# Optimization experiments

Hardware: AMD Instinct MI355X
Metric: run time of the kernel (lower is better)

## Reference

```python
import jax, jax.numpy as jnp
import numpy as np

H = 16      # num_head
DH = 64     # d_head
D = H * DH  # d_model
NEG = -10000.0


def _proj(x, W, b):
    # torch Linear: y = x @ W^T + b
    return jnp.einsum('bld,od->blo', x, W) + b


def _heads(x):
    b, l, _ = x.shape
    return x.reshape(b, l, H, DH)


def _attn_logits(feat_q, mask_q, feat_k, mask_k, Wq, bq, Wk, bk):
    q = _heads(_proj(feat_q, Wq, bq))   # b lq h dh
    k = _heads(_proj(feat_k, Wk, bk))   # b lk h dh
    logits = jnp.einsum('bqhd,bkhd->bhqk', q, k)
    m = mask_q[:, None, :, None] & mask_k[:, None, None, :]  # b 1 lq lk
    return jnp.where(m, logits, NEG)


def setup_inputs() -> dict:
    key = jax.random.key(0)
    ks = jax.random.split(key, 12)
    B, Lv, Lt = 4, 1024, 256
    scale = 1.0 / np.sqrt(D).astype(np.float32)
    inp = {
        'vid_feat': jax.random.normal(ks[0], (B, Lv, D), jnp.float32),
        'vid_mask': jax.random.bernoulli(ks[1], 0.9, (B, Lv)),
        'txt_feat': jax.random.normal(ks[2], (B, Lt, D), jnp.float32),
        'txt_mask': jax.random.bernoulli(ks[3], 0.9, (B, Lt)),
    }
    names = ['v2v', 't2v', 'v2t', 't2t']
    for i, n in enumerate(names):
        inp['W_' + n] = jax.random.normal(ks[4 + i], (3, D, D), jnp.float32) * scale
        inp['b_' + n] = jax.random.normal(ks[8 + i], (3, D), jnp.float32) * 0.01
    return inp


def reference(vid_feat, vid_mask, txt_feat, txt_mask,
              W_v2v, b_v2v, W_t2v, b_t2v, W_v2t, b_v2t, W_t2t, b_t2t):
    B, Lv, _ = vid_feat.shape
    B, Lt, _ = txt_feat.shape
    # sr_ratio == 1: vid_feat_sr == vid_feat, vid_mask_sr == vid_mask
    vid_feat_sr, vid_mask_sr = vid_feat, vid_mask

    # values (proj index 2), concatenated along key length
    v_value = jnp.concatenate([_proj(vid_feat_sr, W_v2v[2], b_v2v[2]),
                               _proj(txt_feat, W_t2v[2], b_t2v[2])], axis=1)
    v_value = _heads(v_value)  # b (Lv+Lt) h dh
    t_value = jnp.concatenate([_proj(vid_feat_sr, W_v2t[2], b_v2t[2]),
                               _proj(txt_feat, W_t2t[2], b_t2t[2])], axis=1)
    t_value = _heads(t_value)

    v2v = _attn_logits(vid_feat, vid_mask, vid_feat_sr, vid_mask_sr,
                       W_v2v[0], b_v2v[0], W_v2v[1], b_v2v[1])
    t2v = _attn_logits(vid_feat, vid_mask, txt_feat, txt_mask,
                       W_t2v[0], b_t2v[0], W_t2v[1], b_t2v[1])
    v2t = _attn_logits(txt_feat, txt_mask, vid_feat_sr, vid_mask_sr,
                       W_v2t[0], b_v2t[0], W_v2t[1], b_v2t[1])
    t2t = _attn_logits(txt_feat, txt_mask, txt_feat, txt_mask,
                       W_t2t[0], b_t2t[0], W_t2t[1], b_t2t[1])

    v_logits = jnp.concatenate([v2v, t2v], axis=-1)  # b h Lv (Lv+Lt)
    t_logits = jnp.concatenate([v2t, t2t], axis=-1)  # b h Lt (Lv+Lt)
    inv_sqrt_dh = jnp.float32(1.0 / np.sqrt(DH))

    # NOTE: original applies softmax, THEN divides by sqrt(d_head) (faithful)
    vid_out = jnp.einsum('bhqk,bkhd->bqhd',
                         jax.nn.softmax(v_logits, axis=-1) * inv_sqrt_dh,
                         v_value).reshape(B, Lv, D)
    txt_out = jnp.einsum('bhqk,bkhd->bqhd',
                         jax.nn.softmax(t_logits, axis=-1) * inv_sqrt_dh,
                         t_value).reshape(B, Lt, D)
    return vid_out, txt_out
```

## Files before the change

### kernel.cpp

```cpp
#include <hip/hip_runtime.h>


typedef __attribute__((ext_vector_type(8))) _Float16  half8;
typedef __attribute__((ext_vector_type(4))) _Float16  half4;
typedef __attribute__((ext_vector_type(4))) float     f32x4;
typedef __attribute__((ext_vector_type(4))) unsigned int uint4v;
typedef __attribute__((ext_vector_type(2))) unsigned int uint2v;

#define MFMA_F16   __builtin_amdgcn_mfma_f32_16x16x32_f16
#define MFMA16_F16 __builtin_amdgcn_mfma_f32_16x16x16f16

static __device__ __forceinline__ unsigned short f_to_f16u(float f) {
  _Float16 h = (_Float16)f;
  return __builtin_bit_cast(unsigned short, h);
}

#define GLOAD_LDS16(g, l)                                            \
  __builtin_amdgcn_global_load_lds(                                  \
      (const __attribute__((address_space(1))) void*)(g),            \
      (__attribute__((address_space(3))) void*)(l), 16, 0, 0)

struct CvtDesc { const float* src; unsigned short* dst; int n8; };
struct CvtArgs { CvtDesc d[14]; };

__global__ __launch_bounds__(256) void cvt_fp16(CvtArgs ca) {
  const CvtDesc dd = ca.d[blockIdx.y];
  const int stride = gridDim.x * blockDim.x;
  for (int i = blockIdx.x * blockDim.x + threadIdx.x; i < dd.n8; i += stride) {
    const f32x4 a = ((const f32x4*)dd.src)[i * 2];
    const f32x4 b = ((const f32x4*)dd.src)[i * 2 + 1];
    half8 h;
    h[0] = (_Float16)a[0]; h[1] = (_Float16)a[1];
    h[2] = (_Float16)a[2]; h[3] = (_Float16)a[3];
    h[4] = (_Float16)b[0]; h[5] = (_Float16)b[1];
    h[6] = (_Float16)b[2]; h[7] = (_Float16)b[3];
    ((half8*)dd.dst)[i] = h;
  }
}

__global__ __launch_bounds__(256) void make_kbias(
    const int* __restrict__ vmask, const int* __restrict__ tmask,
    float* __restrict__ kb) {
  const int b = blockIdx.y;
  const int k = blockIdx.x * 256 + threadIdx.x;
  if (k >= 1280) return;
  const int m = (k < 1024) ? vmask[b * 1024 + k] : tmask[b * 256 + k - 1024];
  kb[b * 1280 + k] = m ? 0.0f : -10000.0f;
}

static __device__ __forceinline__ void copy_out_tile(
    const unsigned short* Cs, unsigned short* dst, int tid,
    int b, int l0, int h0, int Ld, int soff, int mode) {
  for (int i = 0; i < 8; ++i) {
    const int c     = i * 256 + tid;
    const int major = c >> 4;
    const int kc    = c & 15;
    if (mode == 1) {
      const int base = (kc >> 2) * 32 + (kc & 3) * 4;
      const int sw   = major & 7;
      const int o1   = major * 136 + (((base >> 3) ^ sw) << 3) + (base & 7);
      const int b2   = base + 16;
      const int o2   = major * 136 + (((b2 >> 3) ^ sw) << 3) + (b2 & 7);
      const uint2v lo = *(const uint2v*)&Cs[o1];
      const uint2v hi = *(const uint2v*)&Cs[o2];
      uint4v val; val[0] = lo[0]; val[1] = lo[1]; val[2] = hi[0]; val[3] = hi[1];
      const int hh = h0 + (major >> 6);
      const int dh = major & 63;
      const int k  = soff + l0 + (kc >> 2) * 32;
      const size_t el = (size_t)(b * 16 + hh) * 81920 + (size_t)(k >> 5) * 2048 +
                        dh * 32 + (kc & 3) * 8;
      *(uint4v*)(dst + el) = val;
    } else {
      const uint4v val =
          *(const uint4v*)&Cs[major * 136 + ((kc ^ (major & 7)) << 3)];
      if (mode == 0) {
        const size_t el =
            ((size_t)(b * 16 + h0 + (kc >> 3)) * Ld + soff + l0 + major) * 64 +
            (kc & 7) * 8;
        *(uint4v*)(dst + el) = val;
      } else {
        const int k   = soff + l0 + major;
        const int dh0 = (kc & 7) * 8;
        const size_t el = (size_t)(b * 16 + h0 + (kc >> 3)) * 81920 +
                          (size_t)(k >> 4) * 1024 + (dh0 >> 5) * 512 +
                          (k & 15) * 32 + ((dh0 >> 3) & 3) * 8;
        *(uint4v*)(dst + el) = val;
      }
    }
  }
}

struct ProjDescH {
  const unsigned short* X;
  const unsigned short* W;
  const float* Bv;
  unsigned short* dst;
  int M, lxsh, Ld, soff, mode;
};
struct ProjArgsH { ProjDescH d[12]; };

__global__ __launch_bounds__(256) void proj_gemm_h(ProjArgsH pa) {
  const ProjDescH dd = pa.d[blockIdx.z];
  const int m0 = blockIdx.y * 128;
  if (m0 >= dd.M) return;
  const int n0 = blockIdx.x * 128;

  __shared__ __align__(16) unsigned char smem[34816];
  unsigned short* As = (unsigned short*)smem;
  unsigned short* Bs = As + 4096;
  unsigned short* Cs = (unsigned short*)smem;

  const int tid  = threadIdx.x;
  const int lane = tid & 63;
  const int w    = tid >> 6;
  const int wr   = (w >> 1) * 64;
  const int wc   = (w & 1) * 64;
  const int ql   = lane & 15;
  const int qd   = lane >> 4;

  f32x4 acc[4][4];
  for (int i = 0; i < 4; ++i)
    for (int j = 0; j < 4; ++j) acc[i][j] = (f32x4)(0.0f);

  const unsigned short* Xg = dd.X + (size_t)m0 * 1024;
  const unsigned short* Wg = dd.W + (size_t)n0 * 1024;

  for (int k0 = 0; k0 < 1024; k0 += 32) {
    __syncthreads();
    for (int half = 0; half < 2; ++half) {
      const int cb  = w * 128 + half * 64;
      const int c   = cb + lane;
      const int row = c >> 2;
      const int kcg = (c & 3) ^ (row & 3);
      GLOAD_LDS16(Xg + row * 1024 + k0 + kcg * 8, As + cb * 8);
      GLOAD_LDS16(Wg + row * 1024 + k0 + kcg * 8, Bs + cb * 8);
    }
    __syncthreads();

    half8 af[4], bf[4];
    for (int mt = 0; mt < 4; ++mt) {
      const int row = wr + mt * 16 + ql;
      af[mt] = *(const half8*)&As[row * 32 + ((qd ^ (row & 3)) << 3)];
    }
    for (int nt = 0; nt < 4; ++nt) {
      const int row = wc + nt * 16 + ql;
      bf[nt] = *(const half8*)&Bs[row * 32 + ((qd ^ (row & 3)) << 3)];
    }
    for (int mt = 0; mt < 4; ++mt)
      for (int nt = 0; nt < 4; ++nt)
        acc[mt][nt] = MFMA_F16(af[mt], bf[nt], acc[mt][nt], 0, 0, 0);
  }

  float bv[4];
  for (int nt = 0; nt < 4; ++nt)
    bv[nt] = dd.Bv[n0 + wc + nt * 16 + ql];

  __syncthreads();

  for (int mt = 0; mt < 4; ++mt) {
    for (int nt = 0; nt < 4; ++nt) {
      const int nl = wc + nt * 16 + ql;
      for (int r = 0; r < 4; ++r) {
        const int ml = wr + mt * 16 + qd * 4 + r;
        const int row = dd.mode == 1 ? nl : ml;
        const int col = dd.mode == 1 ? ml : nl;
        const float v = acc[mt][nt][r] + bv[nt];
        Cs[row * 136 + (((col >> 3) ^ (row & 7)) << 3) + (col & 7)] = f_to_f16u(v);
      }
    }
  }
  __syncthreads();

  copy_out_tile(Cs, dd.dst, tid, m0 >> dd.lxsh, m0 & ((1 << dd.lxsh) - 1),
                n0 >> 6, dd.Ld, dd.soff, dd.mode);
}

struct ProjDesc {
  const float* X;
  const float* W;
  const float* Bv;
  unsigned short* dst;
  int M, lxsh, Ld, soff, mode;
};
struct ProjArgs { ProjDesc d[12]; };

static __device__ __forceinline__ half8 cvt8sw(const float* base, int row, int g0) {
  const int sw = row & 7;
  const f32x4 a = *(const f32x4*)(base + (row * 8 + (g0 ^ sw)) * 4);
  const f32x4 b = *(const f32x4*)(base + (row * 8 + ((g0 + 1) ^ sw)) * 4);
  half8 h;
  h[0] = (_Float16)a[0]; h[1] = (_Float16)a[1];
  h[2] = (_Float16)a[2]; h[3] = (_Float16)a[3];
  h[4] = (_Float16)b[0]; h[5] = (_Float16)b[1];
  h[6] = (_Float16)b[2]; h[7] = (_Float16)b[3];
  return h;
}

__global__ __launch_bounds__(256) void proj_gemm_f32(ProjArgs pa) {
  const ProjDesc dd = pa.d[blockIdx.z];
  const int m0 = blockIdx.y * 128;
  if (m0 >= dd.M) return;
  const int n0 = blockIdx.x * 128;

  __shared__ __align__(16) unsigned char smem[34816];
  float* As = (float*)smem;
  float* Bs = As + 4096;
  unsigned short* Cs = (unsigned short*)smem;

  const int tid  = threadIdx.x;
  const int lane = tid & 63;
  const int w    = tid >> 6;
  const int wr   = (w >> 1) * 64;
  const int wc   = (w & 1) * 64;
  const int ql   = lane & 15;
  const int qd   = lane >> 4;

  f32x4 acc[4][4];
  for (int i = 0; i < 4; ++i)
    for (int j = 0; j < 4; ++j) acc[i][j] = (f32x4)(0.0f);

  const float* Xg = dd.X + (size_t)m0 * 1024;
  const float* Wg = dd.W + (size_t)n0 * 1024;

  for (int k0 = 0; k0 < 1024; k0 += 32) {
    __syncthreads();
    for (int j = 0; j < 4; ++j) {
      const int cb  = (j * 4 + w) * 64;
      const int c   = cb + lane;
      const int row = c >> 3;
      const int kcg = (c & 7) ^ (row & 7);
      GLOAD_LDS16(Xg + row * 1024 + k0 + kcg * 4, As + cb * 4);
      GLOAD_LDS16(Wg + row * 1024 + k0 + kcg * 4, Bs + cb * 4);
    }
    __syncthreads();

    half8 af[4], bf[4];
    for (int mt = 0; mt < 4; ++mt)
      af[mt] = cvt8sw(As, wr + mt * 16 + ql, qd * 2);
    for (int nt = 0; nt < 4; ++nt)
      bf[nt] = cvt8sw(Bs, wc + nt * 16 + ql, qd * 2);
    for (int mt = 0; mt < 4; ++mt)
      for (int nt = 0; nt < 4; ++nt)
        acc[mt][nt] = MFMA_F16(af[mt], bf[nt], acc[mt][nt], 0, 0, 0);
  }

  float bv[4];
  for (int nt = 0; nt < 4; ++nt)
    bv[nt] = dd.Bv[n0 + wc + nt * 16 + ql];

  __syncthreads();

  for (int mt = 0; mt < 4; ++mt) {
    for (int nt = 0; nt < 4; ++nt) {
      const int nl = wc + nt * 16 + ql;
      for (int r = 0; r < 4; ++r) {
        const int ml = wr + mt * 16 + qd * 4 + r;
        const int row = dd.mode == 1 ? nl : ml;
        const int col = dd.mode == 1 ? ml : nl;
        const float v = acc[mt][nt][r] + bv[nt];
        Cs[row * 136 + (((col >> 3) ^ (row & 7)) << 3) + (col & 7)] = f_to_f16u(v);
      }
    }
  }
  __syncthreads();

  copy_out_tile(Cs, dd.dst, tid, m0 >> dd.lxsh, m0 & ((1 << dd.lxsh) - 1),
                n0 >> 6, dd.Ld, dd.soff, dd.mode);
}

__global__ __launch_bounds__(256) void attn_flash5(
    const unsigned short* __restrict__ Qa_v, const unsigned short* __restrict__ Qb_v,
    const unsigned short* __restrict__ K_v,  const unsigned short* __restrict__ V_vT,
    const unsigned short* __restrict__ Qa_t, const unsigned short* __restrict__ Qb_t,
    const unsigned short* __restrict__ K_t,  const unsigned short* __restrict__ V_tT,
    const int* __restrict__ vmask, const int* __restrict__ tmask,
    const float* __restrict__ kbias,
    float* __restrict__ out_v, float* __restrict__ out_t) {
  __shared__ __align__(16) float oM[4 * 1088];
  __shared__ float mlM[128];

  const bool vside = blockIdx.x < 64;
  const int  qb    = vside ? blockIdx.x : blockIdx.x - 64;
  const int  Lq    = vside ? 1024 : 256;
  const unsigned short* Qa = vside ? Qa_v : Qa_t;
  const unsigned short* Qb = vside ? Qb_v : Qb_t;
  const unsigned short* K  = vside ? K_v  : K_t;
  const unsigned short* VT = vside ? V_vT : V_tT;
  const int* mq  = vside ? vmask : tmask;
  float*     out = vside ? out_v : out_t;

  const int bh = blockIdx.y;
  const int b  = bh >> 4;
  const int h  = bh & 15;
  const int w    = threadIdx.x >> 6;
  const int lane = threadIdx.x & 63;
  const int ql = lane & 15, qd = lane >> 4;
  const int q0 = qb * 16;

  const unsigned short* Qab = Qa + ((size_t)bh * Lq + q0) * 64;
  const unsigned short* Qbb = Qb + ((size_t)bh * Lq + q0) * 64;
  half8 aA[2], aB[2];
  for (int ks = 0; ks < 2; ++ks) {
    aA[ks] = *(const half8*)&Qab[ql * 64 + ks * 32 + qd * 8];
    aB[ks] = *(const half8*)&Qbb[ql * 64 + ks * 32 + qd * 8];
  }
  const int mqs = mq[b * Lq + q0 + ql];

  float m = -1e30f, l = 0.0f;
  f32x4 o[4];
  for (int nt = 0; nt < 4; ++nt) o[nt] = (f32x4)(0.0f);

  const unsigned short* Kb = K  + (size_t)bh * 81920;
  const unsigned short* Vb = VT + (size_t)bh * 81920;
  const float* kbb = kbias + b * 1280;

  const int kw0 = w * 320;
  for (int k0 = kw0; k0 < kw0 + 320; k0 += 32) {
    const bool vidp = (k0 < 1024);

    const unsigned short* Vtile = Vb + (size_t)(k0 >> 5) * 2048;
    half8 vv[4];
    for (int nt = 0; nt < 4; ++nt)
      vv[nt] = *(const half8*)&Vtile[(nt * 16 + ql) * 32 + qd * 8];

    f32x4 sv[2];
    for (int sub = 0; sub < 2; ++sub) {
      const int kb = k0 + sub * 16;
      f32x4 S = *(const f32x4*)&kbb[kb + qd * 4];
      const unsigned short* Ktile = Kb + (size_t)(kb >> 4) * 1024;
      const half8 kf0 = *(const half8*)&Ktile[ql * 32 + qd * 8];
      const half8 kf1 = *(const half8*)&Ktile[512 + ql * 32 + qd * 8];
      if (vidp) { S = MFMA_F16(kf0, aA[0], S, 0, 0, 0); S = MFMA_F16(kf1, aA[1], S, 0, 0, 0); }
      else      { S = MFMA_F16(kf0, aB[0], S, 0, 0, 0); S = MFMA_F16(kf1, aB[1], S, 0, 0, 0); }
      for (int r = 0; r < 4; ++r)
        sv[sub][r] = mqs ? S[r] : -10000.0f;
    }

    float bm = fmaxf(fmaxf(fmaxf(sv[0][0], sv[0][1]), fmaxf(sv[0][2], sv[0][3])),
                     fmaxf(fmaxf(sv[1][0], sv[1][1]), fmaxf(sv[1][2], sv[1][3])));
    bm = fmaxf(bm, __shfl_xor(bm, 16, 64));
    bm = fmaxf(bm, __shfl_xor(bm, 32, 64));
    const float nm = fmaxf(m, bm);
    const float alpha = __expf(m - nm);
    m = nm;
    half4 pv[2];
    float lsum = 0.0f;
    for (int sub = 0; sub < 2; ++sub)
      for (int r = 0; r < 4; ++r) {
        const float p = __expf(sv[sub][r] - m);
        lsum += p;
        pv[sub][r] = (_Float16)p;
      }
    l = l * alpha + lsum;
    for (int nt = 0; nt < 4; ++nt)
      for (int r = 0; r < 4; ++r) o[nt][r] *= alpha;

    for (int nt = 0; nt < 4; ++nt) {
      const half4 vlo = __builtin_shufflevector(vv[nt], vv[nt], 0, 1, 2, 3);
      const half4 vhi = __builtin_shufflevector(vv[nt], vv[nt], 4, 5, 6, 7);
      o[nt] = MFMA16_F16(vlo, pv[0], o[nt], 0, 0, 0);
      o[nt] = MFMA16_F16(vhi, pv[1], o[nt], 0, 0, 0);
    }
  }

  l += __shfl_xor(l, 16, 64);
  l += __shfl_xor(l, 32, 64);

  for (int nt = 0; nt < 4; ++nt)
    for (int r = 0; r < 4; ++r)
      oM[w * 1088 + ql * 68 + nt * 16 + qd * 4 + r] = o[nt][r];
  if (qd == 0) {
    mlM[w * 32 + ql]      = m;
    mlM[w * 32 + 16 + ql] = l;
  }
  __syncthreads();

  const int q  = threadIdx.x >> 4;
  const int d0 = (threadIdx.x & 15) * 4;
  float mw[4], lw[4];
  for (int w2 = 0; w2 < 4; ++w2) {
    mw[w2] = mlM[w2 * 32 + q];
    lw[w2] = mlM[w2 * 32 + 16 + q];
  }
  float ms = fmaxf(fmaxf(mw[0], mw[1]), fmaxf(mw[2], mw[3]));
  float fw[4], ls = 0.0f;
  for (int w2 = 0; w2 < 4; ++w2) {
    fw[w2] = __expf(mw[w2] - ms);
    ls += fw[w2] * lw[w2];
  }
  const float inv = 0.125f / ls;
  f32x4 res;
  for (int j = 0; j < 4; ++j) {
    float a = 0.0f;
    for (int w2 = 0; w2 < 4; ++w2)
      a += fw[w2] * oM[w2 * 1088 + q * 68 + d0 + j];
    res[j] = a * inv;
  }
  *(f32x4*)(out + ((size_t)(b * Lq + q0 + q)) * 1024 + h * 64 + d0) = res;
}

extern "C" void kernel_launch(void* const* d_in, const int* in_sizes, int n_in,
                              void* d_out, int out_size, void* d_ws, size_t ws_size,
                              hipStream_t stream) {
  const float* vid   = (const float*)d_in[0];
  const int*   vmask = (const int*)d_in[1];
  const float* txt   = (const float*)d_in[2];
  const int*   tmask = (const int*)d_in[3];
  const float* Wsrc[4] = {(const float*)d_in[4], (const float*)d_in[6],
                          (const float*)d_in[8], (const float*)d_in[10]};
  const float* Bsrc[4] = {(const float*)d_in[5], (const float*)d_in[7],
                          (const float*)d_in[9], (const float*)d_in[11]};

  const int DD = 1024 * 1024, Dm = 1024, MEG = 1048576;

  unsigned short* ws = (unsigned short*)d_ws;
  unsigned short* Qa_v = ws;
  unsigned short* Qb_v = ws + 4194304;
  unsigned short* K_v  = ws + 8388608;
  unsigned short* V_vT = ws + 13631488;
  unsigned short* Qa_t = ws + 18874368;
  unsigned short* Qb_t = ws + 19922944;
  unsigned short* K_t  = ws + 20971520;
  unsigned short* V_tT = ws + 26214400;
  unsigned short* Xv_h = ws + 31457280;
  unsigned short* Xt_h = ws + 35651584;
  unsigned short* Wh   = ws + 36700160;
  float* kbias = (float*)(ws + 31457280);

  const size_t need = (size_t)49283072 * 2;
  const bool use_h = ws_size >= need;

  if (use_h) {
    CvtArgs ca;
    ca.d[0] = CvtDesc{vid, Xv_h, 4194304 / 8};
    ca.d[1] = CvtDesc{txt, Xt_h, 1048576 / 8};
    for (int s = 0; s < 4; ++s)
      for (int j = 0; j < 3; ++j)
        ca.d[2 + s * 3 + j] = CvtDesc{Wsrc[s] + j * DD, Wh + (s * 3 + j) * MEG, DD / 8};
    cvt_fp16<<<dim3(256, 14), dim3(256), 0, stream>>>(ca);

    ProjArgsH pa;
    auto set = [&](int i, const unsigned short* X, int wi, const float* Bv,
                   unsigned short* dst, int M, int lxsh, int Ld, int soff, int mode) {
      pa.d[i] = ProjDescH{X, Wh + wi * MEG, Bv, dst, M, lxsh, Ld, soff, mode};
    };
    set(0,  Xv_h, 0,  Bsrc[0],          Qa_v, 4096, 10, 1024, 0,    0);
    set(1,  Xv_h, 1,  Bsrc[0] + Dm,     K_v,  4096, 10, 1280, 0,    2);
    set(2,  Xv_h, 2,  Bsrc[0] + 2 * Dm, V_vT, 4096, 10, 1280, 0,    1);
    set(3,  Xv_h, 3,  Bsrc[1],          Qb_v, 4096, 10, 1024, 0,    0);
    set(4,  Xt_h, 4,  Bsrc[1] + Dm,     K_v,  1024, 8,  1280, 1024, 2);
    set(5,  Xt_h, 5,  Bsrc[1] + 2 * Dm, V_vT, 1024, 8,  1280, 1024, 1);
    set(6,  Xt_h, 6,  Bsrc[2],          Qa_t, 1024, 8,  256,  0,    0);
    set(7,  Xv_h, 7,  Bsrc[2] + Dm,     K_t,  4096, 10, 1280, 0,    2);
    set(8,  Xv_h, 8,  Bsrc[2] + 2 * Dm, V_tT, 4096, 10, 1280, 0,    1);
    set(9,  Xt_h, 9,  Bsrc[3],          Qb_t, 1024, 8,  256,  0,    0);
    set(10, Xt_h, 10, Bsrc[3] + Dm,     K_t,  1024, 8,  1280, 1024, 2);
    set(11, Xt_h, 11, Bsrc[3] + 2 * Dm, V_tT, 1024, 8,  1280, 1024, 1);

    proj_gemm_h<<<dim3(8, 32, 12), dim3(256), 0, stream>>>(pa);
  } else {
    ProjArgs pa;
    auto set = [&](int i, const float* X, const float* W, const float* Bv,
                   unsigned short* dst, int M, int lxsh, int Ld, int soff, int mode) {
      pa.d[i] = ProjDesc{X, W, Bv, dst, M, lxsh, Ld, soff, mode};
    };
    set(0,  vid, Wsrc[0],          Bsrc[0],          Qa_v, 4096, 10, 1024, 0,    0);
    set(1,  vid, Wsrc[0] + DD,     Bsrc[0] + Dm,     K_v,  4096, 10, 1280, 0,    2);
    set(2,  vid, Wsrc[0] + 2 * DD, Bsrc[0] + 2 * Dm, V_vT, 4096, 10, 1280, 0,    1);
    set(3,  vid, Wsrc[1],          Bsrc[1],          Qb_v, 4096, 10, 1024, 0,    0);
    set(4,  txt, Wsrc[1] + DD,     Bsrc[1] + Dm,     K_v,  1024, 8,  1280, 1024, 2);
    set(5,  txt, Wsrc[1] + 2 * DD, Bsrc[1] + 2 * Dm, V_vT, 1024, 8,  1280, 1024, 1);
    set(6,  txt, Wsrc[2],          Bsrc[2],          Qa_t, 1024, 8,  256,  0,    0);
    set(7,  vid, Wsrc[2] + DD,     Bsrc[2] + Dm,     K_t,  4096, 10, 1280, 0,    2);
    set(8,  vid, Wsrc[2] + 2 * DD, Bsrc[2] + 2 * Dm, V_tT, 4096, 10, 1280, 0,    1);
    set(9,  txt, Wsrc[3],          Bsrc[3],          Qb_t, 1024, 8,  256,  0,    0);
    set(10, txt, Wsrc[3] + DD,     Bsrc[3] + Dm,     K_t,  1024, 8,  1280, 1024, 2);
    set(11, txt, Wsrc[3] + 2 * DD, Bsrc[3] + 2 * Dm, V_tT, 1024, 8,  1280, 1024, 1);

    proj_gemm_f32<<<dim3(8, 32, 12), dim3(256), 0, stream>>>(pa);
  }

  make_kbias<<<dim3(5, 4), dim3(256), 0, stream>>>(vmask, tmask, kbias);

  float* out_v = (float*)d_out;
  float* out_t = out_v + 4 * 1024 * 1024;
  attn_flash5<<<dim3(80, 64), dim3(256), 0, stream>>>(
      Qa_v, Qb_v, K_v, V_vT, Qa_t, Qb_t, K_t, V_tT,
      vmask, tmask, kbias, out_v, out_t);
}
```

Measured before the change: 332.8 us.

## Share K/V tiles across waves via double-buffered LDS staging in attention

Restructures the attention kernel so each block handles 64 queries, one 16-query slice per wave, and each wave walks the full key range instead of splitting keys across waves. K and V tiles are staged into a swizzled, double-buffered LDS area with async global-to-LDS loads and shared by all four waves, which cuts global/L2 traffic and removes the cross-wave softmax merge. It also skips the rescale when no row max rises, and remaps block IDs across XCDs for locality. The cost is a block barrier every 32 keys and four times fewer blocks in the grid.

```diff
diff --git a/kernel.cpp b/kernel.cpp
--- a/kernel.cpp
+++ b/kernel.cpp
@@ -268,7 +268,7 @@
                 n0 >> 6, dd.Ld, dd.soff, dd.mode);
 }
 
-__global__ __launch_bounds__(256) void attn_flash5(
+__global__ __launch_bounds__(256) void attn_flash6(
     const unsigned short* __restrict__ Qa_v, const unsigned short* __restrict__ Qb_v,
     const unsigned short* __restrict__ K_v,  const unsigned short* __restrict__ V_vT,
     const unsigned short* __restrict__ Qa_t, const unsigned short* __restrict__ Qb_t,
@@ -276,12 +276,16 @@
     const int* __restrict__ vmask, const int* __restrict__ tmask,
     const float* __restrict__ kbias,
     float* __restrict__ out_v, float* __restrict__ out_t) {
-  __shared__ __align__(16) float oM[4 * 1088];
-  __shared__ float mlM[128];
-
-  const bool vside = blockIdx.x < 64;
-  const int  qb    = vside ? blockIdx.x : blockIdx.x - 64;
+  __shared__ __align__(16) unsigned short KVs[8192];
+
+  const int bid = blockIdx.x;
+  const int sid = (bid & 7) * 160 + (bid >> 3);
+  const int bh  = sid / 20;
+  const int sub = sid - bh * 20;
+
+  const bool vside = sub < 16;
   const int  Lq    = vside ? 1024 : 256;
+  const int  qblk  = vside ? sub : sub - 16;
   const unsigned short* Qa = vside ? Qa_v : Qa_t;
   const unsigned short* Qb = vside ? Qb_v : Qb_t;
   const unsigned short* K  = vside ? K_v  : K_t;
@@ -289,13 +293,31 @@
   const int* mq  = vside ? vmask : tmask;
   float*     out = vside ? out_v : out_t;
 
-  const int bh = blockIdx.y;
-  const int b  = bh >> 4;
-  const int h  = bh & 15;
-  const int w    = threadIdx.x >> 6;
-  const int lane = threadIdx.x & 63;
+  const int b = bh >> 4;
+  const int h = bh & 15;
+  const int tid  = threadIdx.x;
+  const int w    = tid >> 6;
+  const int lane = tid & 63;
   const int ql = lane & 15, qd = lane >> 4;
-  const int q0 = qb * 16;
+  const int q0 = qblk * 64 + w * 16;
+
+  const unsigned short* Kb = K  + (size_t)bh * 81920;
+  const unsigned short* Vb = VT + (size_t)bh * 81920;
+  const float* kbb = kbias + b * 1280;
+
+  const int gsw  = (tid ^ ((tid >> 3) & 3)) * 8;
+  const int wlds = w * 512;
+
+#define STAGE6(nb, k0s)                                                     \
+  do {                                                                      \
+    const unsigned short* Kt_ = Kb + (size_t)((k0s) >> 4) * 1024;           \
+    const unsigned short* Vt_ = Vb + (size_t)((k0s) >> 5) * 2048;           \
+    unsigned short* Ld_ = KVs + (nb) * 4096 + wlds;                         \
+    GLOAD_LDS16(Kt_ + gsw, Ld_);                                            \
+    GLOAD_LDS16(Vt_ + gsw, Ld_ + 2048);                                     \
+  } while (0)
+
+  STAGE6(0, 0);
 
   const unsigned short* Qab = Qa + ((size_t)bh * Lq + q0) * 64;
   const unsigned short* Qbb = Qb + ((size_t)bh * Lq + q0) * 64;
@@ -306,54 +328,59 @@
   }
   const int mqs = mq[b * Lq + q0 + ql];
 
+  const int swc = (qd ^ ((ql >> 1) & 3)) * 8;
+
   float m = -1e30f, l = 0.0f;
   f32x4 o[4];
   for (int nt = 0; nt < 4; ++nt) o[nt] = (f32x4)(0.0f);
 
-  const unsigned short* Kb = K  + (size_t)bh * 81920;
-  const unsigned short* Vb = VT + (size_t)bh * 81920;
-  const float* kbb = kbias + b * 1280;
-
-  const int kw0 = w * 320;
-  for (int k0 = kw0; k0 < kw0 + 320; k0 += 32) {
-    const bool vidp = (k0 < 1024);
-
-    const unsigned short* Vtile = Vb + (size_t)(k0 >> 5) * 2048;
+  int cur = 0;
+  for (int t = 0; t < 40; ++t) {
+    __syncthreads();
+    if (t < 39) STAGE6(cur ^ 1, (t + 1) * 32);
+
+    const unsigned short* Ls = KVs + cur * 4096;
+    const int k0 = t * 32;
+    const bool vidp = k0 < 1024;
+
     half8 vv[4];
     for (int nt = 0; nt < 4; ++nt)
-      vv[nt] = *(const half8*)&Vtile[(nt * 16 + ql) * 32 + qd * 8];
+      vv[nt] = *(const half8*)&Ls[2048 + (nt * 16 + ql) * 32 + swc];
 
     f32x4 sv[2];
-    for (int sub = 0; sub < 2; ++sub) {
-      const int kb = k0 + sub * 16;
-      f32x4 S = *(const f32x4*)&kbb[kb + qd * 4];
-      const unsigned short* Ktile = Kb + (size_t)(kb >> 4) * 1024;
-      const half8 kf0 = *(const half8*)&Ktile[ql * 32 + qd * 8];
-      const half8 kf1 = *(const half8*)&Ktile[512 + ql * 32 + qd * 8];
+    for (int s = 0; s < 2; ++s) {
+      f32x4 S = *(const f32x4*)&kbb[k0 + s * 16 + qd * 4];
+      const half8 kf0 = *(const half8*)&Ls[s * 1024 + ql * 32 + swc];
+      const half8 kf1 = *(const half8*)&Ls[s * 1024 + 512 + ql * 32 + swc];
       if (vidp) { S = MFMA_F16(kf0, aA[0], S, 0, 0, 0); S = MFMA_F16(kf1, aA[1], S, 0, 0, 0); }
       else      { S = MFMA_F16(kf0, aB[0], S, 0, 0, 0); S = MFMA_F16(kf1, aB[1], S, 0, 0, 0); }
       for (int r = 0; r < 4; ++r)
-        sv[sub][r] = mqs ? S[r] : -10000.0f;
+        sv[s][r] = mqs ? S[r] : -10000.0f;
     }
 
     float bm = fmaxf(fmaxf(fmaxf(sv[0][0], sv[0][1]), fmaxf(sv[0][2], sv[0][3])),
                      fmaxf(fmaxf(sv[1][0], sv[1][1]), fmaxf(sv[1][2], sv[1][3])));
     bm = fmaxf(bm, __shfl_xor(bm, 16, 64));
     bm = fmaxf(bm, __shfl_xor(bm, 32, 64));
-    const float nm = fmaxf(m, bm);
-    const float alpha = __expf(m - nm);
-    m = nm;
+
+    if (__any(bm > m)) {
+      const float nm = fmaxf(m, bm);
+      const float alpha = __expf(m - nm);
+      l *= alpha;
+      for (int nt = 0; nt < 4; ++nt)
+        for (int r = 0; r < 4; ++r) o[nt][r] *= alpha;
+      m = nm;
+    }
+
     half4 pv[2];
     float lsum = 0.0f;
-    for (int sub = 0; sub < 2; ++sub)
+    for (int s = 0; s < 2; ++s)
       for (int r = 0; r < 4; ++r) {
-        const float p = __expf(sv[sub][r] - m);
+        const float p = __expf(sv[s][r] - m);
         lsum += p;
-        pv[sub][r] = (_Float16)p;
+        pv[s][r] = (_Float16)p;
       }
-    l = l * alpha + lsum;
-    for (int nt = 0; nt < 4; ++nt)
-      for (int r = 0; r < 4; ++r) o[nt][r] *= alpha;
+    l += lsum;
 
     for (int nt = 0; nt < 4; ++nt) {
       const half4 vlo = __builtin_shufflevector(vv[nt], vv[nt], 0, 1, 2, 3);
@@ -361,42 +388,20 @@
       o[nt] = MFMA16_F16(vlo, pv[0], o[nt], 0, 0, 0);
       o[nt] = MFMA16_F16(vhi, pv[1], o[nt], 0, 0, 0);
     }
-  }
+    cur ^= 1;
+  }
+#undef STAGE6
 
   l += __shfl_xor(l, 16, 64);
   l += __shfl_xor(l, 32, 64);
-
-  for (int nt = 0; nt < 4; ++nt)
-    for (int r = 0; r < 4; ++r)
-      oM[w * 1088 + ql * 68 + nt * 16 + qd * 4 + r] = o[nt][r];
-  if (qd == 0) {
-    mlM[w * 32 + ql]      = m;
-    mlM[w * 32 + 16 + ql] = l;
-  }
-  __syncthreads();
-
-  const int q  = threadIdx.x >> 4;
-  const int d0 = (threadIdx.x & 15) * 4;
-  float mw[4], lw[4];
-  for (int w2 = 0; w2 < 4; ++w2) {
-    mw[w2] = mlM[w2 * 32 + q];
-    lw[w2] = mlM[w2 * 32 + 16 + q];
-  }
-  float ms = fmaxf(fmaxf(mw[0], mw[1]), fmaxf(mw[2], mw[3]));
-  float fw[4], ls = 0.0f;
-  for (int w2 = 0; w2 < 4; ++w2) {
-    fw[w2] = __expf(mw[w2] - ms);
-    ls += fw[w2] * lw[w2];
-  }
-  const float inv = 0.125f / ls;
-  f32x4 res;
-  for (int j = 0; j < 4; ++j) {
-    float a = 0.0f;
-    for (int w2 = 0; w2 < 4; ++w2)
-      a += fw[w2] * oM[w2 * 1088 + q * 68 + d0 + j];
-    res[j] = a * inv;
-  }
-  *(f32x4*)(out + ((size_t)(b * Lq + q0 + q)) * 1024 + h * 64 + d0) = res;
+  const float inv = 0.125f / l;
+
+  float* ob = out + ((size_t)(b * Lq + q0 + ql)) * 1024 + h * 64;
+  for (int nt = 0; nt < 4; ++nt) {
+    f32x4 r;
+    for (int j = 0; j < 4; ++j) r[j] = o[nt][j] * inv;
+    *(f32x4*)(ob + nt * 16 + qd * 4) = r;
+  }
 }
 
 extern "C" void kernel_launch(void* const* d_in, const int* in_sizes, int n_in,
@@ -484,7 +489,7 @@
 
   float* out_v = (float*)d_out;
   float* out_t = out_v + 4 * 1024 * 1024;
-  attn_flash5<<<dim3(80, 64), dim3(256), 0, stream>>>(
+  attn_flash6<<<dim3(1280), dim3(256), 0, stream>>>(
       Qa_v, Qb_v, K_v, V_vT, Qa_t, Qb_t, K_t, V_tT,
       vmask, tmask, kbias, out_v, out_t);
 }
```

Result: faster. 309.2 us (-7.1%).
